# Optimization experiments

Measured on AMD Instinct MI355X. Metric: run time of the kernel, lower is better.

## Reference

```python
import jax, jax.numpy as jnp
import numpy as np

EPS = 1e-5


def setup_inputs() -> dict:
    key = jax.random.key(0)
    ks = jax.random.split(key, 11)
    B, Cin, Cout, H, W = 4, 128, 128, 96, 96
    s = 0.05  # small init so offsets stay a few pixels and activations sane
    return {
        'x':     jax.random.normal(ks[0], (B, Cin, H, W), jnp.float32),
        'dw_w':  jax.random.normal(ks[1], (Cin, 1, 3, 3), jnp.float32) * s,   # depthwise 3x3
        'dw_b':  jax.random.normal(ks[2], (Cin,), jnp.float32) * s,
        'pw_w':  jax.random.normal(ks[3], (Cout, Cin), jnp.float32) * s,      # pointwise 1x1
        'pw_b':  jax.random.normal(ks[4], (Cout,), jnp.float32) * s,
        'off_w': jax.random.normal(ks[5], (18, Cout, 3, 3), jnp.float32) * s, # offset conv (2*3*3 ch)
        'off_b': jax.random.normal(ks[6], (18,), jnp.float32) * s,
        'de_w':  jax.random.normal(ks[7], (Cout, Cout, 3, 3), jnp.float32) * s,
        'de_b':  jax.random.normal(ks[8], (Cout,), jnp.float32) * s,
        'gn_w':  jnp.ones((Cout,), jnp.float32),
        'gn_b':  jnp.zeros((Cout,), jnp.float32),
    }


def _conv3x3(x, w, groups=1):
    return jax.lax.conv_general_dilated(
        x, w, (1, 1), ((1, 1), (1, 1)),
        dimension_numbers=('NCHW', 'OIHW', 'NCHW'),
        feature_group_count=groups)


def _deform_conv(x, offset, w, b):
    # torchvision DeformConv2d: 3x3, pad=1, stride=1, dilation=1, 1 offset group.
    # offset layout: [B, 2*9, H, W] with (dy, dx) pairs per kernel tap.
    B, C, H, W = x.shape
    K = 9
    off = offset.reshape(B, K, 2, H, W)
    k = jnp.arange(3, dtype=jnp.float32) - 1.0  # kernel taps relative to center
    ky = jnp.repeat(k, 3)[None, :, None, None]  # [1,K,1,1]
    kx = jnp.tile(k, 3)[None, :, None, None]
    hs = jnp.arange(H, dtype=jnp.float32)[None, None, :, None]
    ws = jnp.arange(W, dtype=jnp.float32)[None, None, None, :]
    py = hs + ky + off[:, :, 0]  # [B,K,H,W] sampling rows
    px = ws + kx + off[:, :, 1]  # [B,K,H,W] sampling cols

    x_hw = x.transpose(0, 2, 3, 1)  # [B,H,W,C] for channel-last gathers
    b_idx = jnp.arange(B)[:, None, None, None]
    y0 = jnp.floor(py)
    x0 = jnp.floor(px)
    ly = py - y0
    lx = px - x0
    y0i = y0.astype(jnp.int32)
    x0i = x0.astype(jnp.int32)

    def corner(yi, xi, wt):
        valid = (yi >= 0) & (yi < H) & (xi >= 0) & (xi < W)  # zero padding
        v = x_hw[b_idx, jnp.clip(yi, 0, H - 1), jnp.clip(xi, 0, W - 1)]  # [B,K,H,W,C]
        return v * (wt * valid)[..., None]

    samp = (corner(y0i,     x0i,     (1 - ly) * (1 - lx))
          + corner(y0i,     x0i + 1, (1 - ly) * lx)
          + corner(y0i + 1, x0i,     ly * (1 - lx))
          + corner(y0i + 1, x0i + 1, ly * lx))  # [B,K,H,W,C]
    out = jnp.einsum('bkhwc,ock->bohw', samp, w.reshape(w.shape[0], C, K))
    return out + b[None, :, None, None]


def reference(x, dw_w, dw_b, pw_w, pw_b, off_w, off_b, de_w, de_b, gn_w, gn_b):
    Cin = x.shape[1]
    # depthwise-separable conv
    h = _conv3x3(x, dw_w, groups=Cin) + dw_b[None, :, None, None]
    h = jnp.einsum('bchw,oc->bohw', h, pw_w) + pw_b[None, :, None, None]
    # InstanceNorm2d (affine=False, biased var)
    mu = h.mean(axis=(2, 3), keepdims=True)
    var = h.var(axis=(2, 3), keepdims=True)
    h = (h - mu) * jax.lax.rsqrt(var + EPS)
    h = jax.nn.relu(h)
    shortcut = h
    # offset conv -> deformable conv
    offset = _conv3x3(h, off_w) + off_b[None, :, None, None]
    d = _deform_conv(h, offset, de_w, de_b)
    # GroupNorm(1, C) with affine
    mu = d.mean(axis=(1, 2, 3), keepdims=True)
    var = d.var(axis=(1, 2, 3), keepdims=True)
    d = (d - mu) * jax.lax.rsqrt(var + EPS)
    d = d * gn_w[None, :, None, None] + gn_b[None, :, None, None]
    g = jax.nn.sigmoid(d)
    return g * shortcut + shortcut
```

## Files before the change

kernel.cpp:

```cpp
#include <hip/hip_runtime.h>
#include <hip/hip_bf16.h>
#include <math.h>

#define B_    4
#define C_    128
#define H_    96
#define W_    96
#define HW_   9216
#define NPIX  36864
#define BHWC  4718592
#define BATCH_STRIDE 1179648

typedef __attribute__((ext_vector_type(8))) short bfrag8;
typedef __attribute__((ext_vector_type(4))) float f32x4;

static __device__ __forceinline__ short f2bf(float f) {
  __hip_bfloat16 h = __float2bfloat16(f);
  short s;
  __builtin_memcpy(&s, &h, 2);
  return s;
}
static __device__ __forceinline__ float bf2f(short s) {
  unsigned u = ((unsigned)(unsigned short)s) << 16;
  float f;
  __builtin_memcpy(&f, &u, 4);
  return f;
}
static __device__ __forceinline__ unsigned cvtpk(float lo, float hi) {
  unsigned r;
  asm("v_cvt_pk_bf16_f32 %0, %1, %2" : "=v"(r) : "v"(lo), "v"(hi));
  return r;
}

__global__ void k_transpose_w(const float* __restrict__ de_w,
                              const float* __restrict__ off_w,
                              const float* __restrict__ pw_w,
                              short* __restrict__ wtb, short* __restrict__ wob,
                              short* __restrict__ pwb) {
  int i = blockIdx.x * 256 + threadIdx.x;
  if (i < 147456) {
    int j  = i & 7;
    int l  = (i >> 3) & 63;
    int kk = (i >> 9) & 3;
    int mt = (i >> 11) & 7;
    int k  = i >> 14;
    int oc = mt * 16 + (l & 15);
    int c  = kk * 32 + ((l >> 4) << 3) + j;
    wtb[i] = f2bf(de_w[(oc * 128 + c) * 9 + k]);
  }
  if (i < 36864) {
    int j  = i & 7;
    int l  = (i >> 3) & 63;
    int kk = (i >> 9) & 3;
    int mt = (i >> 11) & 1;
    int k  = i >> 12;
    int oc = mt * 16 + (l & 15);
    int c  = kk * 32 + ((l >> 4) << 3) + j;
    wob[i] = (oc < 18) ? f2bf(off_w[(oc * 128 + c) * 9 + k]) : (short)0;
  }
  if (i < 16384) {
    int j  = i & 7;
    int l  = (i >> 3) & 63;
    int kk = (i >> 9) & 3;
    int mt = i >> 11;
    int oc = mt * 16 + (l & 15);
    int c  = kk * 32 + ((l >> 4) << 3) + j;
    pwb[i] = f2bf(pw_w[oc * 128 + c]);
  }
}

__global__ void k_dw(const float* __restrict__ x, const float* __restrict__ dw_w,
                     const float* __restrict__ dw_b, float* __restrict__ h1) {
  int i = blockIdx.x * 256 + threadIdx.x;
  if (i >= BHWC) return;
  int xx = i % 96; int yy = (i / 96) % 96; int c = (i / HW_) % 128; int b = i / BATCH_STRIDE;
  const float* xp = x + (b * 128 + c) * HW_;
  const float* wp = dw_w + c * 9;
  float acc = dw_b[c];
  #pragma unroll
  for (int dy = 0; dy < 3; ++dy) {
    int sy = yy + dy - 1;
    if (sy < 0 || sy >= 96) continue;
    #pragma unroll
    for (int dx = 0; dx < 3; ++dx) {
      int sx = xx + dx - 1;
      if (sx < 0 || sx >= 96) continue;
      acc += xp[sy * 96 + sx] * wp[dy * 3 + dx];
    }
  }
  h1[i] = acc;
}

__global__ __launch_bounds__(256) void k_pw(
    const float* __restrict__ h1, const short* __restrict__ pwb,
    const float* __restrict__ pw_b, float* __restrict__ s,
    float* __restrict__ ist) {
  __shared__ short lb[4][4][64][8];
  __shared__ float ps[4][128], pq2[4][128];
  int tid = threadIdx.x;
  int pixbase = blockIdx.x * 64;
  int b = pixbase / HW_;
  int hw0 = pixbase % HW_;

  int pixloc = tid & 63, cq = tid >> 6;
  {
    const float* hp = h1 + (size_t)b * BATCH_STRIDE + hw0 + pixloc;
    #pragma unroll
    for (int it = 0; it < 4; ++it) {
      int c8 = cq * 4 + it;
      int c0 = c8 * 8;
      float v[8];
      #pragma unroll
      for (int j = 0; j < 8; ++j)
        v[j] = hp[(size_t)(c0 + j) * HW_];
      unsigned o0 = cvtpk(v[0], v[1]), o1 = cvtpk(v[2], v[3]);
      unsigned o2 = cvtpk(v[4], v[5]), o3 = cvtpk(v[6], v[7]);
      *(uint4*)&lb[pixloc >> 4][c8 >> 2][(c8 & 3) * 16 + (pixloc & 15)][0] =
          make_uint4(o0, o1, o2, o3);
    }
  }
  __syncthreads();

  int lane = tid & 63, wv = tid >> 6;
  int lp = lane & 15, g = lane >> 4;
  const bfrag8* wp8 = (const bfrag8*)pwb;

  f32x4 acc[8];
  #pragma unroll
  for (int m = 0; m < 8; ++m) acc[m] = (f32x4){0.f, 0.f, 0.f, 0.f};

  #pragma unroll
  for (int kk = 0; kk < 4; ++kk) {
    bfrag8 Bf = *(const bfrag8*)&lb[wv][kk][lane][0];
    #pragma unroll
    for (int m = 0; m < 8; ++m) {
      bfrag8 af = wp8[((size_t)(m * 4 + kk)) * 64 + lane];
      acc[m] = __builtin_amdgcn_mfma_f32_16x16x32_bf16(af, Bf, acc[m], 0, 0, 0);
    }
  }

  int pix = pixbase + wv * 16 + lp;
  #pragma unroll
  for (int m = 0; m < 8; ++m) {
    int oc = m * 16 + g * 4;
    float4 bias = *(const float4*)(pw_b + oc);
    f32x4 a = acc[m];
    float4 v = make_float4(a[0] + bias.x, a[1] + bias.y, a[2] + bias.z, a[3] + bias.w);
    *(float4*)(s + (size_t)pix * 128 + oc) = v;
    float t0 = v.x, t1 = v.y, t2 = v.z, t3 = v.w;
    float u0 = v.x * v.x, u1 = v.y * v.y, u2 = v.z * v.z, u3 = v.w * v.w;
    #pragma unroll
    for (int mask = 1; mask <= 8; mask <<= 1) {
      t0 += __shfl_xor(t0, mask); t1 += __shfl_xor(t1, mask);
      t2 += __shfl_xor(t2, mask); t3 += __shfl_xor(t3, mask);
      u0 += __shfl_xor(u0, mask); u1 += __shfl_xor(u1, mask);
      u2 += __shfl_xor(u2, mask); u3 += __shfl_xor(u3, mask);
    }
    if (lp == 0) {
      ps[wv][oc + 0] = t0; ps[wv][oc + 1] = t1; ps[wv][oc + 2] = t2; ps[wv][oc + 3] = t3;
      pq2[wv][oc + 0] = u0; pq2[wv][oc + 1] = u1; pq2[wv][oc + 2] = u2; pq2[wv][oc + 3] = u3;
    }
  }
  __syncthreads();
  if (tid < 128) {
    float su = ps[0][tid] + ps[1][tid] + ps[2][tid] + ps[3][tid];
    float sq = pq2[0][tid] + pq2[1][tid] + pq2[2][tid] + pq2[3][tid];
    atomicAdd(&ist[(size_t)(b * 128 + tid) * 2],     su);
    atomicAdd(&ist[(size_t)(b * 128 + tid) * 2 + 1], sq);
  }
}

__global__ __launch_bounds__(256) void k_norm(
    const float* __restrict__ s, const float* __restrict__ ist,
    short* __restrict__ nsamp) {
  int t = blockIdx.x * 256 + threadIdx.x;
  int pix = t >> 4; int c0 = (t & 15) * 8;
  int b = pix / HW_;
  const float* sp = s + (size_t)pix * 128 + c0;
  float4 a0 = *(const float4*)sp, a1 = *(const float4*)(sp + 4);
  float v[8] = {a0.x, a0.y, a0.z, a0.w, a1.x, a1.y, a1.z, a1.w};
  bfrag8 o;
  #pragma unroll
  for (int j = 0; j < 8; ++j) {
    size_t ci = (size_t)(b * 128 + c0 + j) * 2;
    float mean = ist[ci] * (1.f / 9216.f);
    float var  = ist[ci + 1] * (1.f / 9216.f) - mean * mean;
    float rs = rsqrtf(var + 1e-5f);
    o[j] = f2bf(fmaxf((v[j] - mean) * rs, 0.f));
  }
  *(bfrag8*)(nsamp + (size_t)pix * 128 + c0) = o;
}

__global__ __launch_bounds__(256) void k_offgemm(
    const short* __restrict__ nsamp, const short* __restrict__ wob,
    const float* __restrict__ off_b, float* __restrict__ off) {
  int tid = threadIdx.x;
  int lane = tid & 63, wv = tid >> 6;
  int p0 = blockIdx.x * 128 + wv * 32;
  int lp = lane & 15, g = lane >> 4;
  const bfrag8* np = (const bfrag8*)nsamp;
  const bfrag8* wp = (const bfrag8*)wob;

  f32x4 acc[2][2];
  #pragma unroll
  for (int m = 0; m < 2; ++m)
    #pragma unroll
    for (int n = 0; n < 2; ++n) acc[m][n] = (f32x4){0.f, 0.f, 0.f, 0.f};

  int pn0 = p0 + lp, pn1 = p0 + 16 + lp;
  int x0_ = pn0 % 96, y0_ = (pn0 % HW_) / 96;
  int x1_ = pn1 % 96, y1_ = (pn1 % HW_) / 96;
  const bfrag8 zf = {0, 0, 0, 0, 0, 0, 0, 0};

  for (int k = 0; k < 9; ++k) {
    int dy = k / 3 - 1, dx = k % 3 - 1;
    int sh = dy * 96 + dx;
    bool v0 = ((unsigned)(x0_ + dx) < 96u) && ((unsigned)(y0_ + dy) < 96u);
    bool v1 = ((unsigned)(x1_ + dx) < 96u) && ((unsigned)(y1_ + dy) < 96u);
    int q0 = min(max(pn0 + sh, 0), NPIX - 1);
    int q1 = min(max(pn1 + sh, 0), NPIX - 1);
    size_t a0 = (size_t)q0 * 16 + g;
    size_t a1 = (size_t)q1 * 16 + g;
    #pragma unroll
    for (int kk = 0; kk < 4; ++kk) {
      bfrag8 B0 = np[a0 + kk * 4]; B0 = v0 ? B0 : zf;
      bfrag8 B1 = np[a1 + kk * 4]; B1 = v1 ? B1 : zf;
      bfrag8 A0 = wp[((size_t)(k * 2 + 0) * 4 + kk) * 64 + lane];
      bfrag8 A1 = wp[((size_t)(k * 2 + 1) * 4 + kk) * 64 + lane];
      acc[0][0] = __builtin_amdgcn_mfma_f32_16x16x32_bf16(A0, B0, acc[0][0], 0, 0, 0);
      acc[0][1] = __builtin_amdgcn_mfma_f32_16x16x32_bf16(A0, B1, acc[0][1], 0, 0, 0);
      acc[1][0] = __builtin_amdgcn_mfma_f32_16x16x32_bf16(A1, B0, acc[1][0], 0, 0, 0);
      acc[1][1] = __builtin_amdgcn_mfma_f32_16x16x32_bf16(A1, B1, acc[1][1], 0, 0, 0);
    }
  }

  #pragma unroll
  for (int mt = 0; mt < 2; ++mt) {
    #pragma unroll
    for (int r = 0; r < 4; ++r) {
      int oc = mt * 16 + g * 4 + r;
      if (oc < 18) {
        float bb = off_b[oc];
        off[(size_t)oc * NPIX + p0 + lp]      = acc[mt][0][r] + bb;
        off[(size_t)oc * NPIX + p0 + 16 + lp] = acc[mt][1][r] + bb;
      }
    }
  }
}

__global__ __launch_bounds__(256) void k_deform_f(
    const short* __restrict__ nsamp, const float* __restrict__ off,
    const short* __restrict__ wtb, const float* __restrict__ de_b,
    float* __restrict__ d, float* __restrict__ gst) {
  __shared__ short lbuf[2][2][16][17][8];
  __shared__ float offl[18][32];
  __shared__ float r1[256], r2[256];
  int tid = threadIdx.x;
  int bid = blockIdx.x;
  int wg = (bid & 7) * 144 + (bid >> 3);
  int pixbase = wg * 32;

  int lane = tid & 63, wv = tid >> 6;
  int lp = lane & 15, g = lane >> 4;
  int pq = lane >> 4, ch = lane & 15;

  #pragma unroll
  for (int t = 0; t < 3; ++t) {
    int i = t * 256 + tid;
    if (i < 576)
      offl[i >> 5][i & 31] = off[(size_t)(i >> 5) * NPIX + pixbase + (i & 31)];
  }
  __syncthreads();

  int lpixA[2], ysA[2], xsA[2], qbA[2];
  #pragma unroll
  for (int q = 0; q < 2; ++q) {
    int lpix = wv * 8 + q * 4 + pq;
    int pix = pixbase + lpix;
    int hw = pix % HW_;
    lpixA[q] = lpix;
    ysA[q] = hw / 96;
    xsA[q] = hw % 96;
    qbA[q] = (pix / HW_) * HW_;
  }

  int mtg0 = wv * 2;
  const bfrag8* wp = (const bfrag8*)wtb;

  f32x4 acc[2][2];
  #pragma unroll
  for (int m = 0; m < 2; ++m)
    #pragma unroll
    for (int n = 0; n < 2; ++n) acc[m][n] = (f32x4){0.f, 0.f, 0.f, 0.f};

  bfrag8 cs0[2][4], cs1[2][4];

  auto ISSUE = [&](int k, bfrag8 (&cs)[2][4]) {
    #pragma unroll
    for (int q = 0; q < 2; ++q) {
      float dy = offl[2 * k][lpixA[q]];
      float dx = offl[2 * k + 1][lpixA[q]];
      float py = (float)ysA[q] + (float)(k / 3 - 1) + dy;
      float px = (float)xsA[q] + (float)(k % 3 - 1) + dx;
      int y0 = (int)floorf(py), x0 = (int)floorf(px);
      int yc0 = min(max(y0, 0), 95), yc1 = min(max(y0 + 1, 0), 95);
      int xc0 = min(max(x0, 0), 95), xc1 = min(max(x0 + 1, 0), 95);
      const short* base = nsamp + (size_t)ch * 8;
      cs[q][0] = *(const bfrag8*)(base + (size_t)(qbA[q] + yc0 * 96 + xc0) * 128);
      cs[q][1] = *(const bfrag8*)(base + (size_t)(qbA[q] + yc0 * 96 + xc1) * 128);
      cs[q][2] = *(const bfrag8*)(base + (size_t)(qbA[q] + yc1 * 96 + xc0) * 128);
      cs[q][3] = *(const bfrag8*)(base + (size_t)(qbA[q] + yc1 * 96 + xc1) * 128);
    }
  };

  auto FINISH = [&](int k, bfrag8 (&cs)[2][4], int buf) {
    #pragma unroll
    for (int q = 0; q < 2; ++q) {
      float dy = offl[2 * k][lpixA[q]];
      float dx = offl[2 * k + 1][lpixA[q]];
      float py = (float)ysA[q] + (float)(k / 3 - 1) + dy;
      float px = (float)xsA[q] + (float)(k % 3 - 1) + dx;
      float y0f = floorf(py), x0f = floorf(px);
      float ly = py - y0f, lx = px - x0f;
      int y0 = (int)y0f, x0 = (int)x0f;
      bool vy0 = (y0 >= 0) && (y0 < 96), vy1 = (y0 + 1 >= 0) && (y0 + 1 < 96);
      bool vx0 = (x0 >= 0) && (x0 < 96), vx1 = (x0 + 1 >= 0) && (x0 + 1 < 96);
      float w00 = (vy0 && vx0) ? (1.f - ly) * (1.f - lx) : 0.f;
      float w01 = (vy0 && vx1) ? (1.f - ly) * lx : 0.f;
      float w10 = (vy1 && vx0) ? ly * (1.f - lx) : 0.f;
      float w11 = (vy1 && vx1) ? ly * lx : 0.f;
      float v[8];
      #pragma unroll
      for (int j = 0; j < 8; ++j) {
        v[j] = bf2f(cs[q][0][j]) * w00 + bf2f(cs[q][1][j]) * w01
             + bf2f(cs[q][2][j]) * w10 + bf2f(cs[q][3][j]) * w11;
      }
      unsigned o0 = cvtpk(v[0], v[1]), o1 = cvtpk(v[2], v[3]);
      unsigned o2 = cvtpk(v[4], v[5]), o3 = cvtpk(v[6], v[7]);
      int lpix = lpixA[q];
      *(uint4*)&lbuf[buf][lpix >> 4][lpix & 15][ch][0] = make_uint4(o0, o1, o2, o3);
    }
  };

  ISSUE(0, cs0);
  #pragma unroll
  for (int k = 0; k < 9; ++k) {
    if (k < 8) {
      if ((k + 1) & 1) ISSUE(k + 1, cs1);
      else             ISSUE(k + 1, cs0);
    }
    if (k & 1) FINISH(k, cs1, 1);
    else       FINISH(k, cs0, 0);
    __syncthreads();
    int cur = k & 1;
    #pragma unroll
    for (int kk = 0; kk < 4; ++kk) {
      bfrag8 B0 = *(const bfrag8*)&lbuf[cur][0][lp][kk * 4 + g][0];
      bfrag8 B1 = *(const bfrag8*)&lbuf[cur][1][lp][kk * 4 + g][0];
      #pragma unroll
      for (int m = 0; m < 2; ++m) {
        bfrag8 af = wp[((size_t)((k * 8 + mtg0 + m) * 4 + kk)) * 64 + lane];
        acc[m][0] = __builtin_amdgcn_mfma_f32_16x16x32_bf16(af, B0, acc[m][0], 0, 0, 0);
        acc[m][1] = __builtin_amdgcn_mfma_f32_16x16x32_bf16(af, B1, acc[m][1], 0, 0, 0);
      }
    }
  }

  float lsum = 0.f, lsq = 0.f;
  #pragma unroll
  for (int m = 0; m < 2; ++m) {
    int oc = (mtg0 + m) * 16 + g * 4;
    float4 bias = *(const float4*)(de_b + oc);
    #pragma unroll
    for (int n = 0; n < 2; ++n) {
      int pix = pixbase + n * 16 + lp;
      f32x4 a = acc[m][n];
      float4 v = make_float4(a[0] + bias.x, a[1] + bias.y, a[2] + bias.z, a[3] + bias.w);
      *(float4*)(d + (size_t)pix * 128 + oc) = v;
      lsum += v.x + v.y + v.z + v.w;
      lsq  += v.x * v.x + v.y * v.y + v.z * v.z + v.w * v.w;
    }
  }
  __syncthreads();
  r1[tid] = lsum; r2[tid] = lsq;
  __syncthreads();
  for (int st = 128; st > 0; st >>= 1) {
    if (tid < st) { r1[tid] += r1[tid + st]; r2[tid] += r2[tid + st]; }
    __syncthreads();
  }
  if (tid == 0) {
    int b = pixbase / HW_;
    atomicAdd(&gst[b * 2],     r1[0]);
    atomicAdd(&gst[b * 2 + 1], r2[0]);
  }
}

__global__ __launch_bounds__(256) void k_final(
    const float* __restrict__ d, const short* __restrict__ nsamp,
    const float* __restrict__ gst, const float* __restrict__ gn_w,
    const float* __restrict__ gn_b, float* __restrict__ out) {
  __shared__ float t[128 * 33];
  int tid = threadIdx.x;
  int pixbase = blockIdx.x * 32;
  int b = pixbase / HW_;
  int hw0 = pixbase % HW_;
  const float invN = 1.f / (float)BATCH_STRIDE;
  float gm = gst[2 * b] * invN;
  float gr = rsqrtf(gst[2 * b + 1] * invN - gm * gm + 1e-5f);

  int px0 = tid >> 3;
  int c0  = (tid & 7) * 16;
  const float* dp = d + ((size_t)(pixbase + px0)) * 128;
  const short* np = nsamp + ((size_t)(pixbase + px0)) * 128 + c0;
  bfrag8 sv0 = *(const bfrag8*)np;
  bfrag8 sv1 = *(const bfrag8*)(np + 8);
  #pragma unroll
  for (int q = 0; q < 4; ++q) {
    int c = c0 + q * 4;
    float4 dv = *(const float4*)(dp + c);
    float4 w4 = *(const float4*)(gn_w + c);
    float4 b4 = *(const float4*)(gn_b + c);
    #pragma unroll
    for (int e = 0; e < 4; ++e) {
      int idx = q * 4 + e;
      float svn = bf2f(idx < 8 ? sv0[idx & 7] : sv1[idx & 7]);
      float dvx = e == 0 ? dv.x : (e == 1 ? dv.y : (e == 2 ? dv.z : dv.w));
      float wx  = e == 0 ? w4.x : (e == 1 ? w4.y : (e == 2 ? w4.z : w4.w));
      float bx  = e == 0 ? b4.x : (e == 1 ? b4.y : (e == 2 ? b4.z : b4.w));
      float dn = (dvx - gm) * gr * wx + bx;
      float gg = 1.f / (1.f + expf(-dn));
      t[(c + e) * 33 + px0] = svn * (1.f + gg);
    }
  }
  __syncthreads();
  if (tid < 128) {
    float* op = out + (size_t)(b * 128 + tid) * HW_ + hw0;
    #pragma unroll
    for (int p4 = 0; p4 < 8; ++p4) {
      float4 v = make_float4(t[tid * 33 + p4 * 4], t[tid * 33 + p4 * 4 + 1],
                             t[tid * 33 + p4 * 4 + 2], t[tid * 33 + p4 * 4 + 3]);
      *(float4*)(op + p4 * 4) = v;
    }
  }
}

extern "C" void kernel_launch(void* const* d_in, const int* in_sizes, int n_in,
                              void* d_out, int out_size, void* d_ws, size_t ws_size,
                              hipStream_t stream) {
  (void)in_sizes; (void)n_in; (void)out_size; (void)ws_size;
  const float* x     = (const float*)d_in[0];
  const float* dw_w  = (const float*)d_in[1];
  const float* dw_b  = (const float*)d_in[2];
  const float* pw_w  = (const float*)d_in[3];
  const float* pw_b  = (const float*)d_in[4];
  const float* off_w = (const float*)d_in[5];
  const float* off_b = (const float*)d_in[6];
  const float* de_w  = (const float*)d_in[7];
  const float* de_b  = (const float*)d_in[8];
  const float* gn_w  = (const float*)d_in[9];
  const float* gn_b  = (const float*)d_in[10];
  float* out = (float*)d_out;

  float* ws   = (float*)d_ws;
  float* h1   = ws;
  float* s    = h1 + BHWC;
  float* off  = s + BHWC;
  short* wtb  = (short*)(off + NPIX * 18);
  short* wob  = wtb + 147456;
  short* pwb  = wob + 36864;
  float* ist  = (float*)(pwb + 16384);
  float* gst  = ist + 1024;
  short* nsamp = (short*)(gst + 8);

  hipMemsetAsync(ist, 0, (1024 + 8) * sizeof(float), stream);

  k_transpose_w<<<576, 256, 0, stream>>>(de_w, off_w, pw_w, wtb, wob, pwb);
  k_dw<<<BHWC / 256, 256, 0, stream>>>(x, dw_w, dw_b, h1);
  k_pw<<<NPIX / 64, 256, 0, stream>>>(h1, pwb, pw_b, s, ist);
  k_norm<<<NPIX * 16 / 256, 256, 0, stream>>>(s, ist, nsamp);
  k_offgemm<<<NPIX / 128, 256, 0, stream>>>(nsamp, wob, off_b, off);
  k_deform_f<<<NPIX / 32, 256, 0, stream>>>(nsamp, off, wtb, de_b, h1, gst);
  k_final<<<NPIX / 32, 256, 0, stream>>>(h1, nsamp, gst, gn_w, gn_b, out);
}
```

Baseline: 165.3 us.

## Fuse depthwise conv into pointwise GEMM and store intermediates as bf16

The depthwise 3x3 convolution now runs inside the pointwise MFMA kernel's staging loop, which removes the separate k_dw launch and the fp32 h1 round trip through global memory. The pre-norm pointwise output and the deformable conv output are now written and read as bf16 instead of fp32, which halves that traffic. The cost is nine gathered loads per channel inside k_pw and lower precision in the values that feed the norm statistics and the final gate, which could affect accuracy.

```diff
diff --git a/kernel.cpp b/kernel.cpp
--- a/kernel.cpp
+++ b/kernel.cpp
@@ -69,31 +69,10 @@
   }
 }
 
-__global__ void k_dw(const float* __restrict__ x, const float* __restrict__ dw_w,
-                     const float* __restrict__ dw_b, float* __restrict__ h1) {
-  int i = blockIdx.x * 256 + threadIdx.x;
-  if (i >= BHWC) return;
-  int xx = i % 96; int yy = (i / 96) % 96; int c = (i / HW_) % 128; int b = i / BATCH_STRIDE;
-  const float* xp = x + (b * 128 + c) * HW_;
-  const float* wp = dw_w + c * 9;
-  float acc = dw_b[c];
-  #pragma unroll
-  for (int dy = 0; dy < 3; ++dy) {
-    int sy = yy + dy - 1;
-    if (sy < 0 || sy >= 96) continue;
-    #pragma unroll
-    for (int dx = 0; dx < 3; ++dx) {
-      int sx = xx + dx - 1;
-      if (sx < 0 || sx >= 96) continue;
-      acc += xp[sy * 96 + sx] * wp[dy * 3 + dx];
-    }
-  }
-  h1[i] = acc;
-}
-
 __global__ __launch_bounds__(256) void k_pw(
-    const float* __restrict__ h1, const short* __restrict__ pwb,
-    const float* __restrict__ pw_b, float* __restrict__ s,
+    const float* __restrict__ x, const float* __restrict__ dw_w,
+    const float* __restrict__ dw_b, const short* __restrict__ pwb,
+    const float* __restrict__ pw_b, short* __restrict__ sbf,
     float* __restrict__ ist) {
   __shared__ short lb[4][4][64][8];
   __shared__ float ps[4][128], pq2[4][128];
@@ -104,15 +83,38 @@
 
   int pixloc = tid & 63, cq = tid >> 6;
   {
-    const float* hp = h1 + (size_t)b * BATCH_STRIDE + hw0 + pixloc;
+    int hw = hw0 + pixloc;
+    int y = hw / 96, xx = hw % 96;
+    const float* xb = x + (size_t)b * 128 * HW_;
+    int toff[9];
+    float tmask[9];
+    #pragma unroll
+    for (int dy = 0; dy < 3; ++dy) {
+      #pragma unroll
+      for (int dx = 0; dx < 3; ++dx) {
+        int sy = y + dy - 1, sx = xx + dx - 1;
+        bool vld = ((unsigned)sy < 96u) && ((unsigned)sx < 96u);
+        int syc = min(max(sy, 0), 95), sxc = min(max(sx, 0), 95);
+        toff[dy * 3 + dx] = syc * 96 + sxc;
+        tmask[dy * 3 + dx] = vld ? 1.f : 0.f;
+      }
+    }
     #pragma unroll
     for (int it = 0; it < 4; ++it) {
       int c8 = cq * 4 + it;
       int c0 = c8 * 8;
       float v[8];
       #pragma unroll
-      for (int j = 0; j < 8; ++j)
-        v[j] = hp[(size_t)(c0 + j) * HW_];
+      for (int j = 0; j < 8; ++j) {
+        int c = c0 + j;
+        const float* xp = xb + (size_t)c * HW_;
+        const float* wp = dw_w + c * 9;
+        float a = dw_b[c];
+        #pragma unroll
+        for (int t9 = 0; t9 < 9; ++t9)
+          a = fmaf(xp[toff[t9]] * tmask[t9], wp[t9], a);
+        v[j] = a;
+      }
       unsigned o0 = cvtpk(v[0], v[1]), o1 = cvtpk(v[2], v[3]);
       unsigned o2 = cvtpk(v[4], v[5]), o3 = cvtpk(v[6], v[7]);
       *(uint4*)&lb[pixloc >> 4][c8 >> 2][(c8 & 3) * 16 + (pixloc & 15)][0] =
@@ -146,7 +148,7 @@
     float4 bias = *(const float4*)(pw_b + oc);
     f32x4 a = acc[m];
     float4 v = make_float4(a[0] + bias.x, a[1] + bias.y, a[2] + bias.z, a[3] + bias.w);
-    *(float4*)(s + (size_t)pix * 128 + oc) = v;
+    *(uint2*)(sbf + (size_t)pix * 128 + oc) = make_uint2(cvtpk(v.x, v.y), cvtpk(v.z, v.w));
     float t0 = v.x, t1 = v.y, t2 = v.z, t3 = v.w;
     float u0 = v.x * v.x, u1 = v.y * v.y, u2 = v.z * v.z, u3 = v.w * v.w;
     #pragma unroll
@@ -171,14 +173,12 @@
 }
 
 __global__ __launch_bounds__(256) void k_norm(
-    const float* __restrict__ s, const float* __restrict__ ist,
+    const short* __restrict__ sbf, const float* __restrict__ ist,
     short* __restrict__ nsamp) {
   int t = blockIdx.x * 256 + threadIdx.x;
   int pix = t >> 4; int c0 = (t & 15) * 8;
   int b = pix / HW_;
-  const float* sp = s + (size_t)pix * 128 + c0;
-  float4 a0 = *(const float4*)sp, a1 = *(const float4*)(sp + 4);
-  float v[8] = {a0.x, a0.y, a0.z, a0.w, a1.x, a1.y, a1.z, a1.w};
+  bfrag8 sv = *(const bfrag8*)(sbf + (size_t)pix * 128 + c0);
   bfrag8 o;
   #pragma unroll
   for (int j = 0; j < 8; ++j) {
@@ -186,7 +186,7 @@
     float mean = ist[ci] * (1.f / 9216.f);
     float var  = ist[ci + 1] * (1.f / 9216.f) - mean * mean;
     float rs = rsqrtf(var + 1e-5f);
-    o[j] = f2bf(fmaxf((v[j] - mean) * rs, 0.f));
+    o[j] = f2bf(fmaxf((bf2f(sv[j]) - mean) * rs, 0.f));
   }
   *(bfrag8*)(nsamp + (size_t)pix * 128 + c0) = o;
 }
@@ -251,7 +251,7 @@
 __global__ __launch_bounds__(256) void k_deform_f(
     const short* __restrict__ nsamp, const float* __restrict__ off,
     const short* __restrict__ wtb, const float* __restrict__ de_b,
-    float* __restrict__ d, float* __restrict__ gst) {
+    short* __restrict__ d, float* __restrict__ gst) {
   __shared__ short lbuf[2][2][16][17][8];
   __shared__ float offl[18][32];
   __shared__ float r1[256], r2[256];
@@ -376,7 +376,7 @@
       int pix = pixbase + n * 16 + lp;
       f32x4 a = acc[m][n];
       float4 v = make_float4(a[0] + bias.x, a[1] + bias.y, a[2] + bias.z, a[3] + bias.w);
-      *(float4*)(d + (size_t)pix * 128 + oc) = v;
+      *(uint2*)(d + (size_t)pix * 128 + oc) = make_uint2(cvtpk(v.x, v.y), cvtpk(v.z, v.w));
       lsum += v.x + v.y + v.z + v.w;
       lsq  += v.x * v.x + v.y * v.y + v.z * v.z + v.w * v.w;
     }
@@ -396,7 +396,7 @@
 }
 
 __global__ __launch_bounds__(256) void k_final(
-    const float* __restrict__ d, const short* __restrict__ nsamp,
+    const short* __restrict__ d, const short* __restrict__ nsamp,
     const float* __restrict__ gst, const float* __restrict__ gn_w,
     const float* __restrict__ gn_b, float* __restrict__ out) {
   __shared__ float t[128 * 33];
@@ -410,21 +410,22 @@
 
   int px0 = tid >> 3;
   int c0  = (tid & 7) * 16;
-  const float* dp = d + ((size_t)(pixbase + px0)) * 128;
+  const short* dp = d + ((size_t)(pixbase + px0)) * 128 + c0;
   const short* np = nsamp + ((size_t)(pixbase + px0)) * 128 + c0;
+  bfrag8 dv0 = *(const bfrag8*)dp;
+  bfrag8 dv1 = *(const bfrag8*)(dp + 8);
   bfrag8 sv0 = *(const bfrag8*)np;
   bfrag8 sv1 = *(const bfrag8*)(np + 8);
   #pragma unroll
   for (int q = 0; q < 4; ++q) {
     int c = c0 + q * 4;
-    float4 dv = *(const float4*)(dp + c);
     float4 w4 = *(const float4*)(gn_w + c);
     float4 b4 = *(const float4*)(gn_b + c);
     #pragma unroll
     for (int e = 0; e < 4; ++e) {
       int idx = q * 4 + e;
+      float dvx = bf2f(idx < 8 ? dv0[idx & 7] : dv1[idx & 7]);
       float svn = bf2f(idx < 8 ? sv0[idx & 7] : sv1[idx & 7]);
-      float dvx = e == 0 ? dv.x : (e == 1 ? dv.y : (e == 2 ? dv.z : dv.w));
       float wx  = e == 0 ? w4.x : (e == 1 ? w4.y : (e == 2 ? w4.z : w4.w));
       float bx  = e == 0 ? b4.x : (e == 1 ? b4.y : (e == 2 ? b4.z : b4.w));
       float dn = (dvx - gm) * gr * wx + bx;
@@ -462,23 +463,22 @@
   float* out = (float*)d_out;
 
   float* ws   = (float*)d_ws;
-  float* h1   = ws;
-  float* s    = h1 + BHWC;
-  float* off  = s + BHWC;
+  float* off  = ws;
   short* wtb  = (short*)(off + NPIX * 18);
   short* wob  = wtb + 147456;
   short* pwb  = wob + 36864;
   float* ist  = (float*)(pwb + 16384);
   float* gst  = ist + 1024;
-  short* nsamp = (short*)(gst + 8);
+  short* sbf  = (short*)(gst + 8);
+  short* dbf  = sbf + (size_t)NPIX * 128;
+  short* nsamp = dbf + (size_t)NPIX * 128;
 
   hipMemsetAsync(ist, 0, (1024 + 8) * sizeof(float), stream);
 
   k_transpose_w<<<576, 256, 0, stream>>>(de_w, off_w, pw_w, wtb, wob, pwb);
-  k_dw<<<BHWC / 256, 256, 0, stream>>>(x, dw_w, dw_b, h1);
-  k_pw<<<NPIX / 64, 256, 0, stream>>>(h1, pwb, pw_b, s, ist);
-  k_norm<<<NPIX * 16 / 256, 256, 0, stream>>>(s, ist, nsamp);
+  k_pw<<<NPIX / 64, 256, 0, stream>>>(x, dw_w, dw_b, pwb, pw_b, sbf, ist);
+  k_norm<<<NPIX * 16 / 256, 256, 0, stream>>>(sbf, ist, nsamp);
   k_offgemm<<<NPIX / 128, 256, 0, stream>>>(nsamp, wob, off_b, off);
-  k_deform_f<<<NPIX / 32, 256, 0, stream>>>(nsamp, off, wtb, de_b, h1, gst);
-  k_final<<<NPIX / 32, 256, 0, stream>>>(h1, nsamp, gst, gn_w, gn_b, out);
-}
+  k_deform_f<<<NPIX / 32, 256, 0, stream>>>(nsamp, off, wtb, de_b, dbf, gst);
+  k_final<<<NPIX / 32, 256, 0, stream>>>(dbf, nsamp, gst, gn_w, gn_b, out);
+}
```

Result: faster. 138.8 us (median of 2 runs) (-16.1%).
